# Performance work log

Measured on AMD Instinct MI355X. Metric: run time of the kernel, lower is better.

The kernel has to match this reference:

```python
import jax, jax.numpy as jnp
import numpy as np

EMB_DIM = 1024
SEQ = 2048
BATCH = 4


def setup_inputs() -> dict:
    key = jax.random.key(0)
    k1, k2, k3, k4, k5 = jax.random.split(key, 5)
    Q = jax.random.normal(k1, (SEQ, BATCH, EMB_DIM), dtype=jnp.float32)
    K = jax.random.normal(k2, (SEQ, BATCH, EMB_DIM), dtype=jnp.float32)
    V = jax.random.normal(k3, (SEQ, BATCH, EMB_DIM), dtype=jnp.float32)
    # nn.Linear default init scale ~ 1/sqrt(fan_in)
    W_in = jax.random.normal(k4, (3 * EMB_DIM, EMB_DIM), dtype=jnp.float32) / np.sqrt(EMB_DIM)
    W_out = jax.random.normal(k5, (EMB_DIM, EMB_DIM), dtype=jnp.float32) / np.sqrt(EMB_DIM)
    return {"Q": Q, "K": K, "V": V, "W_in": W_in, "W_out": W_out}


def reference(Q, K, V, W_in, W_out):
    # NOTE: original module ignores K and V args entirely (self-attention on Q).
    emb = Q.shape[-1]
    scale = 1.0 / np.sqrt(emb)
    qkv = jnp.einsum('sbe,fe->sbf', Q, W_in)        # [S, B, 3E]
    q, k, v = jnp.split(qkv, 3, axis=-1)            # each [S, B, E]
    q = jnp.transpose(q, (1, 0, 2)) * scale         # [B, S, E]
    k = jnp.transpose(k, (1, 0, 2))                 # [B, S, E]
    v = jnp.transpose(v, (1, 0, 2))                 # [B, S, E]
    scores = jnp.einsum('bte,bse->bts', q, k)       # [B, T, S]
    # per-target-row softmax over source dim == vectorized softmax on last axis
    weights = jax.nn.softmax(scores, axis=-1)       # [B, T, S]
    out = jnp.einsum('bts,bse->bte', weights, v)    # [B, T, E]
    out = jnp.transpose(out, (1, 0, 2))             # [T, B, E]
    out = jnp.einsum('tbe,fe->tbf', out, W_out)     # [T, B, E]
    return (out, weights)
```

## Files before the change

### kernel.cpp

```cpp
#include <hip/hip_runtime.h>
#include <stdint.h>

typedef unsigned short u16;
typedef __bf16 bf16_t;
typedef bf16_t bf16x8 __attribute__((ext_vector_type(8)));
typedef float f32x4 __attribute__((ext_vector_type(4)));
typedef u16 u16x4 __attribute__((ext_vector_type(4)));
typedef u16 u16x8 __attribute__((ext_vector_type(8)));

#define AS1 __attribute__((address_space(1)))
#define AS3 __attribute__((address_space(3)))

__device__ __forceinline__ u16 f2bf(float f) {
  union { float f; uint32_t u; } x; x.f = f;
  uint32_t u = x.u;
  return (u16)((u + 0x7fffu + ((u >> 16) & 1u)) >> 16);
}

__device__ __forceinline__ float bf2f(u16 b) {
  union { uint32_t u; float f; } x; x.u = ((uint32_t)b) << 16;
  return x.f;
}

__device__ __forceinline__ void gload_lds16(const void* g, void* lds) {
  __builtin_amdgcn_global_load_lds((const AS1 uint32_t*)g, (AS3 uint32_t*)lds, 16, 0, 0);
}

__global__ __launch_bounds__(256) void cvt_bf16(const float* __restrict__ in,
                                                u16* __restrict__ out, int n4) {
  int i = blockIdx.x * 256 + threadIdx.x;
  if (i >= n4) return;
  float4 v = ((const float4*)in)[i];
  u16x4 o = {f2bf(v.x), f2bf(v.y), f2bf(v.z), f2bf(v.w)};
  *(u16x4*)(out + (size_t)i * 4) = o;
}

#define BARRIER() do { asm volatile("" ::: "memory"); \
                       __builtin_amdgcn_s_barrier();  \
                       asm volatile("" ::: "memory"); } while (0)

#define MQS(MQi, NQi, ASET, BSET)                                              \
  do {                                                                         \
    __builtin_amdgcn_s_setprio(1);                                             \
    _Pragma("unroll") for (int j_ = 0; j_ < 4; ++j_) {                         \
      _Pragma("unroll") for (int i_ = 0; i_ < 2; ++i_) {                       \
        acc[(MQi) * 4 + j_][(NQi) * 2 + i_] =                                  \
            __builtin_amdgcn_mfma_f32_16x16x32_bf16(                           \
                ASET[j_][0], BSET[i_][0],                                      \
                acc[(MQi) * 4 + j_][(NQi) * 2 + i_], 0, 0, 0);                 \
        acc[(MQi) * 4 + j_][(NQi) * 2 + i_] =                                  \
            __builtin_amdgcn_mfma_f32_16x16x32_bf16(                           \
                ASET[j_][1], BSET[i_][1],                                      \
                acc[(MQi) * 4 + j_][(NQi) * 2 + i_], 0, 0, 0);                 \
      }                                                                        \
    }                                                                          \
    __builtin_amdgcn_s_setprio(0);                                             \
  } while (0)

template <bool BF16OUT>
__global__ __launch_bounds__(512, 2)
void gemm256(const u16* __restrict__ A, const u16* __restrict__ B,
             void* __restrict__ Cv,
             int lda, int ldb, int ldc,
             long long sAz, long long sBz, long long sCz,
             int K, float alpha) {
  __shared__ u16 As[2][256 * 64];
  __shared__ u16 Bs[2][256 * 64];
  const int tid  = threadIdx.x;
  const int lane = tid & 63;
  const int wid  = tid >> 6;
  const int wr   = wid >> 2;
  const int wc   = wid & 3;
  const long long z = blockIdx.z;
  const u16* Ab = A + z * sAz;
  const u16* Bb = B + z * sBz;
  const int rowBase = blockIdx.y * 256;
  const int colBase = blockIdx.x * 256;
  const int nt = K >> 6;

  const int sRow   = tid >> 3;
  const int sChunk = (tid & 7) ^ (sRow & 7);
  const size_t ldaS = (size_t)lda, ldbS = (size_t)ldb;
  const u16* aS = Ab + (size_t)(rowBase + sRow) * ldaS + sChunk * 8;
  const u16* bS = Bb + (size_t)(colBase + sRow) * ldbS + sChunk * 8;

  const int fr = lane & 15;
  const int kx = lane >> 4;
  const int rx = lane & 7;

  f32x4 acc[8][4];
  const f32x4 zf = {0.f, 0.f, 0.f, 0.f};
#pragma unroll
  for (int m = 0; m < 8; ++m)
#pragma unroll
    for (int n = 0; n < 4; ++n) acc[m][n] = zf;

  bf16x8 Ara[4][2], Arb[4][2], Bra[2][2], Brb[2][2];

  auto stageA = [&](int buf, int h, int kt) {
    const u16* s = aS + (size_t)(h * 128) * ldaS + kt;
    char* d = ((char*)&As[buf][0]) + h * 16384 + tid * 16;
    gload_lds16(s, d);
    gload_lds16(s + 64 * ldaS, d + 8192);
  };
  auto stageB = [&](int buf, int h, int kt) {
    const u16* s = bS + (size_t)(h * 128) * ldbS + kt;
    char* d = ((char*)&Bs[buf][0]) + h * 16384 + tid * 16;
    gload_lds16(s, d);
    gload_lds16(s + 64 * ldbS, d + 8192);
  };
  auto ldsA = [&](int buf, int mq, bf16x8 (&dst)[4][2]) {
#pragma unroll
    for (int j = 0; j < 4; ++j) {
      const int row = mq * 128 + wr * 64 + j * 16 + fr;
#pragma unroll
      for (int k = 0; k < 2; ++k) {
        const int ch = ((k * 4 + kx) ^ rx) * 8;
        dst[j][k] = *(const bf16x8*)&As[buf][row * 64 + ch];
      }
    }
  };
  auto ldsB = [&](int buf, int nq, bf16x8 (&dst)[2][2]) {
#pragma unroll
    for (int i = 0; i < 2; ++i) {
      const int row = nq * 128 + i * 64 + wc * 16 + fr;
#pragma unroll
      for (int k = 0; k < 2; ++k) {
        const int ch = ((k * 4 + kx) ^ rx) * 8;
        dst[i][k] = *(const bf16x8*)&Bs[buf][row * 64 + ch];
      }
    }
  };

  stageA(0, 0, 0);
  stageA(0, 1, 0);
  stageB(0, 0, 0);
  stageB(0, 1, 0);
  asm volatile("s_waitcnt vmcnt(0)" ::: "memory");
  BARRIER();
  ldsA(0, 0, Ara);
  ldsB(0, 0, Bra);

  for (int t = 0; t < nt; ++t) {
    const int c = t & 1;
    const int kt1 = (t + 1) << 6;
    const bool s1 = (t + 1 < nt);
    ldsB(c, 1, Brb);
    ldsA(c, 1, Arb);
    if (s1) {
      stageA(1 - c, 0, kt1);
      stageA(1 - c, 1, kt1);
      stageB(1 - c, 0, kt1);
      stageB(1 - c, 1, kt1);
    }
    MQS(0, 0, Ara, Bra);
    MQS(0, 1, Ara, Brb);
    if (s1) {
      asm volatile("s_waitcnt lgkmcnt(0)" ::: "memory");
      asm volatile("s_waitcnt vmcnt(0)" ::: "memory");
      BARRIER();
      ldsA(1 - c, 0, Ara);
      __builtin_amdgcn_sched_barrier(0);
    }
    MQS(1, 0, Arb, Bra);
    if (s1) ldsB(1 - c, 0, Bra);
    MQS(1, 1, Arb, Brb);
  }

  const int r0 = (lane >> 4) * 4;
#pragma unroll
  for (int m = 0; m < 8; ++m) {
    const int grow = rowBase + (m >> 2) * 128 + wr * 64 + (m & 3) * 16 + r0;
#pragma unroll
    for (int jj = 0; jj < 4; ++jj) {
      const size_t rOff = (size_t)(grow + jj) * (size_t)ldc;
      if constexpr (BF16OUT) {
        u16* C = (u16*)Cv + z * sCz;
#pragma unroll
        for (int n = 0; n < 4; ++n) {
          const int gcol = colBase + (n >> 1) * 128 + (n & 1) * 64 + wc * 16 + fr;
          C[rOff + gcol] = f2bf(acc[m][n][jj] * alpha);
        }
      } else {
        float* C = (float*)Cv + z * sCz;
#pragma unroll
        for (int n = 0; n < 4; ++n) {
          const int gcol = colBase + (n >> 1) * 128 + (n & 1) * 64 + wc * 16 + fr;
          C[rOff + gcol] = acc[m][n][jj] * alpha;
        }
      }
    }
  }
}

template <bool BF16OUT>
__global__ __launch_bounds__(512, 2)
void gemm128(const u16* __restrict__ A, const u16* __restrict__ B,
             void* __restrict__ Cv,
             int lda, int ldb, int ldc,
             long long sAz, long long sBz, long long sCz,
             int K, float alpha) {
  __shared__ u16 As[2][128 * 64];
  __shared__ u16 Bs[2][256 * 64];
  const int tid  = threadIdx.x;
  const int lane = tid & 63;
  const int wid  = tid >> 6;
  const int wr   = wid >> 2;
  const int wc   = wid & 3;
  const long long z = blockIdx.z;
  const u16* Ab = A + z * sAz;
  const u16* Bb = B + z * sBz;
  const int rowBase = blockIdx.y * 128;
  const int colBase = blockIdx.x * 256;
  const int nt = K >> 6;

  const int sRow   = tid >> 3;
  const int sChunk = (tid & 7) ^ (sRow & 7);
  const size_t ldaS = (size_t)lda, ldbS = (size_t)ldb;
  const u16* aS = Ab + (size_t)(rowBase + sRow) * ldaS + sChunk * 8;
  const u16* bS = Bb + (size_t)(colBase + sRow) * ldbS + sChunk * 8;

  const int fr = lane & 15;
  const int kx = lane >> 4;
  const int rx = lane & 7;

  f32x4 acc[4][4];
  const f32x4 zf = {0.f, 0.f, 0.f, 0.f};
#pragma unroll
  for (int m = 0; m < 4; ++m)
#pragma unroll
    for (int n = 0; n < 4; ++n) acc[m][n] = zf;

  bf16x8 Ara[4][2], Arb[4][2], Bra[2][2], Brb[2][2];

  auto stageA = [&](int buf, int kt) {
    const u16* s = aS + kt;
    char* d = ((char*)&As[buf][0]) + tid * 16;
    gload_lds16(s, d);
    gload_lds16(s + 64 * ldaS, d + 8192);
  };
  auto stageB = [&](int buf, int h, int kt) {
    const u16* s = bS + (size_t)(h * 128) * ldbS + kt;
    char* d = ((char*)&Bs[buf][0]) + h * 16384 + tid * 16;
    gload_lds16(s, d);
    gload_lds16(s + 64 * ldbS, d + 8192);
  };
  auto ldsA = [&](int buf, bf16x8 (&dst)[4][2]) {
#pragma unroll
    for (int j = 0; j < 4; ++j) {
      const int row = wr * 64 + j * 16 + fr;
#pragma unroll
      for (int k = 0; k < 2; ++k) {
        const int ch = ((k * 4 + kx) ^ rx) * 8;
        dst[j][k] = *(const bf16x8*)&As[buf][row * 64 + ch];
      }
    }
  };
  auto ldsB = [&](int buf, int nq, bf16x8 (&dst)[2][2]) {
#pragma unroll
    for (int i = 0; i < 2; ++i) {
      const int row = nq * 128 + i * 64 + wc * 16 + fr;
#pragma unroll
      for (int k = 0; k < 2; ++k) {
        const int ch = ((k * 4 + kx) ^ rx) * 8;
        dst[i][k] = *(const bf16x8*)&Bs[buf][row * 64 + ch];
      }
    }
  };

  auto tile = [&](int t, int c, bf16x8 (&ACUR)[4][2], bf16x8 (&ANXT)[4][2]) {
    const int kt1 = (t + 1) << 6;
    const bool s1 = (t + 1 < nt);
    ldsB(c, 1, Brb);
    if (s1) {
      stageA(1 - c, kt1);
      stageB(1 - c, 0, kt1);
      stageB(1 - c, 1, kt1);
    }
    MQS(0, 0, ACUR, Bra);
    if (s1) {
      asm volatile("s_waitcnt lgkmcnt(0)" ::: "memory");
      asm volatile("s_waitcnt vmcnt(0)" ::: "memory");
      BARRIER();
      ldsA(1 - c, ANXT);
      ldsB(1 - c, 0, Bra);
      __builtin_amdgcn_sched_barrier(0);
    }
    MQS(0, 1, ACUR, Brb);
  };

  stageA(0, 0);
  stageB(0, 0, 0);
  stageB(0, 1, 0);
  asm volatile("s_waitcnt vmcnt(0)" ::: "memory");
  BARRIER();
  ldsA(0, Ara);
  ldsB(0, 0, Bra);

  for (int tt = 0; tt < nt; tt += 2) {
    tile(tt,     0, Ara, Arb);
    tile(tt + 1, 1, Arb, Ara);
  }

  const int r0 = (lane >> 4) * 4;
#pragma unroll
  for (int m = 0; m < 4; ++m) {
    const int grow = rowBase + wr * 64 + m * 16 + r0;
#pragma unroll
    for (int jj = 0; jj < 4; ++jj) {
      const size_t rOff = (size_t)(grow + jj) * (size_t)ldc;
      if constexpr (BF16OUT) {
        u16* C = (u16*)Cv + z * sCz;
#pragma unroll
        for (int n = 0; n < 4; ++n) {
          const int gcol = colBase + (n >> 1) * 128 + (n & 1) * 64 + wc * 16 + fr;
          C[rOff + gcol] = f2bf(acc[m][n][jj] * alpha);
        }
      } else {
        float* C = (float*)Cv + z * sCz;
#pragma unroll
        for (int n = 0; n < 4; ++n) {
          const int gcol = colBase + (n >> 1) * 128 + (n & 1) * 64 + wc * 16 + fr;
          C[rOff + gcol] = acc[m][n][jj] * alpha;
        }
      }
    }
  }
}

__global__ __launch_bounds__(256)
void softmax_rows(u16* __restrict__ sbf, float* __restrict__ wfp) {
  const size_t row = blockIdx.x;
  const int tid = threadIdx.x;
  u16* pb = sbf + row * 2048;
  u16x8 xb = *(const u16x8*)(pb + tid * 8);
  float x[8];
#pragma unroll
  for (int j = 0; j < 8; ++j) x[j] = bf2f(xb[j]);
  float m = x[0];
#pragma unroll
  for (int j = 1; j < 8; ++j) m = fmaxf(m, x[j]);
#pragma unroll
  for (int o = 32; o; o >>= 1) m = fmaxf(m, __shfl_xor(m, o, 64));
  __shared__ float red[8];
  if ((tid & 63) == 0) red[tid >> 6] = m;
  __syncthreads();
  m = fmaxf(fmaxf(red[0], red[1]), fmaxf(red[2], red[3]));
  float e[8];
  float s = 0.f;
#pragma unroll
  for (int j = 0; j < 8; ++j) { e[j] = expf(x[j] - m); s += e[j]; }
#pragma unroll
  for (int o = 32; o; o >>= 1) s += __shfl_xor(s, o, 64);
  if ((tid & 63) == 0) red[4 + (tid >> 6)] = s;
  __syncthreads();
  s = (red[4] + red[5]) + (red[6] + red[7]);
  const float inv = 1.0f / s;
  float w[8];
#pragma unroll
  for (int j = 0; j < 8; ++j) w[j] = e[j] * inv;
  float* pf = wfp + row * 2048;
  float4 o0 = {w[0], w[1], w[2], w[3]};
  float4 o1 = {w[4], w[5], w[6], w[7]};
  ((float4*)pf)[tid * 2] = o0;
  ((float4*)pf)[tid * 2 + 1] = o1;
  u16x8 ub;
#pragma unroll
  for (int j = 0; j < 8; ++j) ub[j] = f2bf(w[j]);
  *(u16x8*)(pb + tid * 8) = ub;
}

extern "C" void kernel_launch(void* const* d_in, const int* in_sizes, int n_in,
                              void* d_out, int out_size, void* d_ws, size_t ws_size,
                              hipStream_t stream) {
  const float* Q  = (const float*)d_in[0];
  const float* Wi = (const float*)d_in[3];
  const float* Wo = (const float*)d_in[4];
  float* out0    = (float*)d_out;
  float* weights = out0 + (size_t)2048 * 4 * 1024;

  char* ws = (char*)d_ws;
  u16* Qb   = (u16*)(ws);
  u16* Wib  = (u16*)(ws + ((size_t)16 << 20));
  u16* Wob  = (u16*)(ws + ((size_t)22 << 20));
  u16* qkvb = (u16*)(ws + ((size_t)24 << 20));
  u16* vwT  = (u16*)(ws + ((size_t)72 << 20));
  u16* wbf  = (u16*)(ws + ((size_t)88 << 20));

  cvt_bf16<<<dim3(8192), dim3(256), 0, stream>>>(Q,  Qb,  2097152);
  cvt_bf16<<<dim3(3072), dim3(256), 0, stream>>>(Wi, Wib, 786432);
  cvt_bf16<<<dim3(1024), dim3(256), 0, stream>>>(Wo, Wob, 262144);

  gemm256<true><<<dim3(8, 32, 1), dim3(512), 0, stream>>>(
      Qb, Wib, (void*)qkvb, 1024, 1024, 3072, 0, 0, 0, 1024, 1.0f);

  gemm128<true><<<dim3(4, 64, 1), dim3(512), 0, stream>>>(
      Qb, Wib + (size_t)2048 * 1024, (void*)(qkvb + 2048),
      1024, 1024, 3072, 0, 0, 0, 1024, 1.0f);

  gemm256<true><<<dim3(8, 8, 4), dim3(512), 0, stream>>>(
      qkvb, qkvb + 1024, (void*)wbf, 12288, 12288, 2048,
      3072LL, 3072LL, 4194304LL, 1024, 0.03125f);

  gemm128<true><<<dim3(8, 8, 4), dim3(512), 0, stream>>>(
      Wob, qkvb + 2048, (void*)vwT, 1024, 12288, 2048,
      0LL, 3072LL, 2097152LL, 1024, 1.0f);

  softmax_rows<<<dim3(8192), dim3(256), 0, stream>>>(wbf, weights);

  gemm128<false><<<dim3(4, 16, 4), dim3(512), 0, stream>>>(
      wbf, vwT, (void*)out0, 2048, 2048, 4096,
      4194304LL, 2097152LL, 1024LL, 2048, 1.0f);
}
```

Measured before the change: 211.6 us.

## Load B operand fragments directly from global into registers, bypassing LDS

In the gemm128 kernel the B tile no longer goes through shared memory. Each wave now loads its MFMA B fragments straight from global memory into double-buffered registers, one k-tile ahead. This removes the LDS footprint and LDS traffic for B, which could raise occupancy and cut LDS bandwidth pressure. In exchange, B rows shared by waves in the same column group are fetched redundantly from global or L2, the per-lane loads are less coalesced, and register pressure grows under launch_bounds(512,2).

```diff
diff --git a/kernel.cpp b/kernel.cpp
--- a/kernel.cpp
+++ b/kernel.cpp
@@ -201,7 +201,6 @@
              long long sAz, long long sBz, long long sCz,
              int K, float alpha) {
   __shared__ u16 As[2][128 * 64];
-  __shared__ u16 Bs[2][256 * 64];
   const int tid  = threadIdx.x;
   const int lane = tid & 63;
   const int wid  = tid >> 6;
@@ -218,7 +217,6 @@
   const int sChunk = (tid & 7) ^ (sRow & 7);
   const size_t ldaS = (size_t)lda, ldbS = (size_t)ldb;
   const u16* aS = Ab + (size_t)(rowBase + sRow) * ldaS + sChunk * 8;
-  const u16* bS = Bb + (size_t)(colBase + sRow) * ldbS + sChunk * 8;
 
   const int fr = lane & 15;
   const int kx = lane >> 4;
@@ -231,7 +229,8 @@
 #pragma unroll
     for (int n = 0; n < 4; ++n) acc[m][n] = zf;
 
-  bf16x8 Ara[4][2], Arb[4][2], Bra[2][2], Brb[2][2];
+  bf16x8 Ara[4][2], Arb[4][2];
+  bf16x8 B0a[2][2], B1a[2][2], B0b[2][2], B1b[2][2];
 
   auto stageA = [&](int buf, int kt) {
     const u16* s = aS + kt;
@@ -239,12 +238,6 @@
     gload_lds16(s, d);
     gload_lds16(s + 64 * ldaS, d + 8192);
   };
-  auto stageB = [&](int buf, int h, int kt) {
-    const u16* s = bS + (size_t)(h * 128) * ldbS + kt;
-    char* d = ((char*)&Bs[buf][0]) + h * 16384 + tid * 16;
-    gload_lds16(s, d);
-    gload_lds16(s + 64 * ldbS, d + 8192);
-  };
   auto ldsA = [&](int buf, bf16x8 (&dst)[4][2]) {
 #pragma unroll
     for (int j = 0; j < 4; ++j) {
@@ -256,50 +249,53 @@
       }
     }
   };
-  auto ldsB = [&](int buf, int nq, bf16x8 (&dst)[2][2]) {
+  auto gloadB = [&](bf16x8 (&dst)[2][2], int nq, int kt) {
 #pragma unroll
     for (int i = 0; i < 2; ++i) {
-      const int row = nq * 128 + i * 64 + wc * 16 + fr;
+      const u16* src =
+          Bb + (size_t)(colBase + nq * 128 + i * 64 + wc * 16 + fr) * ldbS + kt;
 #pragma unroll
       for (int k = 0; k < 2; ++k) {
-        const int ch = ((k * 4 + kx) ^ rx) * 8;
-        dst[i][k] = *(const bf16x8*)&Bs[buf][row * 64 + ch];
-      }
-    }
-  };
-
-  auto tile = [&](int t, int c, bf16x8 (&ACUR)[4][2], bf16x8 (&ANXT)[4][2]) {
+        dst[i][k] = *(const bf16x8*)(src + (k * 4 + kx) * 8);
+      }
+    }
+  };
+
+  auto tile = [&](int t, int c, bf16x8 (&ACUR)[4][2], bf16x8 (&ANXT)[4][2],
+                  bf16x8 (&BC0)[2][2], bf16x8 (&BC1)[2][2],
+                  bf16x8 (&BN0)[2][2], bf16x8 (&BN1)[2][2]) {
     const int kt1 = (t + 1) << 6;
     const bool s1 = (t + 1 < nt);
-    ldsB(c, 1, Brb);
     if (s1) {
       stageA(1 - c, kt1);
-      stageB(1 - c, 0, kt1);
-      stageB(1 - c, 1, kt1);
-    }
-    MQS(0, 0, ACUR, Bra);
+      __builtin_amdgcn_sched_barrier(0);
+      gloadB(BN0, 0, kt1);
+      gloadB(BN1, 1, kt1);
+      __builtin_amdgcn_sched_barrier(0);
+    }
+    MQS(0, 0, ACUR, BC0);
     if (s1) {
       asm volatile("s_waitcnt lgkmcnt(0)" ::: "memory");
       asm volatile("s_waitcnt vmcnt(0)" ::: "memory");
       BARRIER();
       ldsA(1 - c, ANXT);
-      ldsB(1 - c, 0, Bra);
       __builtin_amdgcn_sched_barrier(0);
     }
-    MQS(0, 1, ACUR, Brb);
+    MQS(0, 1, ACUR, BC1);
   };
 
   stageA(0, 0);
-  stageB(0, 0, 0);
-  stageB(0, 1, 0);
+  __builtin_amdgcn_sched_barrier(0);
+  gloadB(B0a, 0, 0);
+  gloadB(B1a, 1, 0);
   asm volatile("s_waitcnt vmcnt(0)" ::: "memory");
+  __builtin_amdgcn_sched_barrier(0);
   BARRIER();
   ldsA(0, Ara);
-  ldsB(0, 0, Bra);
 
   for (int tt = 0; tt < nt; tt += 2) {
-    tile(tt,     0, Ara, Arb);
-    tile(tt + 1, 1, Arb, Ara);
+    tile(tt,     0, Ara, Arb, B0a, B1a, B0b, B1b);
+    tile(tt + 1, 1, Arb, Ara, B0b, B1b, B0a, B1a);
   }
 
   const int r0 = (lane >> 4) * 4;
```

Result: slower. 289.5 us (+36.8%).
